# Kernel tuning notes

Hardware: AMD Instinct MI355X
Metric: run time of the kernel (lower is better)

The kernel has to match this reference:

```python
import jax, jax.numpy as jnp
import numpy as np
import math

D_MODEL, N_HEADS, D_FF = 1024, 16, 4096
D_K = D_MODEL // N_HEADS
B, S = 4, 2048
EPS = 1e-5


def layer_norm(x, gamma, beta):
    mean = jnp.mean(x, axis=-1, keepdims=True)
    var = jnp.mean((x - mean) ** 2, axis=-1, keepdims=True)  # unbiased=False
    return gamma * (x - mean) / jnp.sqrt(var + EPS) + beta


def setup_inputs() -> dict:
    key = jax.random.key(0)
    ks = jax.random.split(key, 7)
    std_attn = math.sqrt(2.0 / (D_MODEL + D_MODEL))
    std_ff1 = math.sqrt(2.0 / (D_MODEL + D_FF))
    std_ff2 = math.sqrt(2.0 / (D_FF + D_MODEL))
    return {
        "x": jax.random.normal(ks[0], (B, S, D_MODEL), jnp.float32),
        "W_q": jax.random.normal(ks[1], (D_MODEL, D_MODEL), jnp.float32) * std_attn,
        "W_k": jax.random.normal(ks[2], (D_MODEL, D_MODEL), jnp.float32) * std_attn,
        "W_v": jax.random.normal(ks[3], (D_MODEL, D_MODEL), jnp.float32) * std_attn,
        "W_o": jax.random.normal(ks[4], (D_MODEL, D_MODEL), jnp.float32) * std_attn,
        "W1": jax.random.normal(ks[5], (D_MODEL, D_FF), jnp.float32) * std_ff1,
        "b1": jnp.zeros((D_FF,), jnp.float32),
        "W2": jax.random.normal(ks[6], (D_FF, D_MODEL), jnp.float32) * std_ff2,
        "b2": jnp.zeros((D_MODEL,), jnp.float32),
        "ln1_gamma": jnp.ones((D_MODEL,), jnp.float32),
        "ln1_beta": jnp.zeros((D_MODEL,), jnp.float32),
        "ln2_gamma": jnp.ones((D_MODEL,), jnp.float32),
        "ln2_beta": jnp.zeros((D_MODEL,), jnp.float32),
    }


def reference(x, W_q, W_k, W_v, W_o, W1, b1, W2, b2,
              ln1_gamma, ln1_beta, ln2_gamma, ln2_beta):
    b, s, d = x.shape
    # pre-LN attention block
    ln1 = layer_norm(x, ln1_gamma, ln1_beta)
    q = (ln1 @ W_q).reshape(b, s, N_HEADS, D_K)
    k = (ln1 @ W_k).reshape(b, s, N_HEADS, D_K)
    v = (ln1 @ W_v).reshape(b, s, N_HEADS, D_K)
    scores = jnp.einsum("bqhd,bkhd->bhqk", q, k) / math.sqrt(D_K)
    attn = jax.nn.softmax(scores, axis=-1)
    ctx = jnp.einsum("bhqk,bkhd->bqhd", attn, v).reshape(b, s, d)
    attn_out = ctx @ W_o
    attn_residual = x + attn_out
    # pre-LN FFN block
    ln2 = layer_norm(attn_residual, ln2_gamma, ln2_beta)
    ff = jax.nn.relu(ln2 @ W1 + b1) @ W2 + b2
    return attn_residual + ff
```

## Files before the change

kernel.cpp:

```cpp
#include <hip/hip_runtime.h>
#include <hip/hip_bf16.h>

typedef __attribute__((ext_vector_type(4)))  float  floatx4;
typedef __attribute__((ext_vector_type(16))) float  floatx16;
typedef __attribute__((ext_vector_type(8)))  short  shortx8;
typedef __attribute__((ext_vector_type(4)))  short  shortx4;

__device__ __forceinline__ short f2bf(float f) {
    unsigned u = __float_as_uint(f);
    u += 0x7fffu + ((u >> 16) & 1u);
    return (short)(u >> 16);
}
__device__ __forceinline__ float bf2f(short s) {
    return __uint_as_float(((unsigned)(unsigned short)s) << 16);
}
__device__ __forceinline__ float fast_exp2(float x) {
#if __has_builtin(__builtin_amdgcn_exp2f)
    return __builtin_amdgcn_exp2f(x);
#else
    return exp2f(x);
#endif
}

__device__ __forceinline__ void load_lds16(const void* g, void* l) {
    __builtin_amdgcn_global_load_lds(
        (const __attribute__((address_space(1))) unsigned int*)g,
        (__attribute__((address_space(3))) unsigned int*)l,
        16, 0, 0);
}

__global__ __launch_bounds__(256)
void transpose_w(const float* __restrict__ src, short* __restrict__ dst, int K, int N)
{
    __shared__ __align__(16) float tile[32][33];
    const int n0 = blockIdx.x * 32, k0 = blockIdx.y * 32;
    const int tx = threadIdx.x & 31, ty = threadIdx.x >> 5;
    for (int i = 0; i < 32; i += 8)
        tile[ty + i][tx] = src[(size_t)(k0 + ty + i) * N + n0 + tx];
    __syncthreads();
    for (int i = 0; i < 32; i += 8)
        dst[(size_t)(n0 + ty + i) * K + k0 + tx] = f2bf(tile[tx][ty + i]);
}

__global__ __launch_bounds__(256)
void ln_bf16(const float* __restrict__ x, const float* __restrict__ g,
             const float* __restrict__ be, short* __restrict__ out)
{
    const int row = blockIdx.x;
    const int tid = threadIdx.x;
    const float4 v = reinterpret_cast<const float4*>(x + (size_t)row * 1024)[tid];
    float s  = v.x + v.y + v.z + v.w;
    float ss = v.x * v.x + v.y * v.y + v.z * v.z + v.w * v.w;
    for (int off = 32; off > 0; off >>= 1) {
        s  += __shfl_down(s,  off);
        ss += __shfl_down(ss, off);
    }
    __shared__ float rs[4], rss[4];
    const int wave = tid >> 6, lane = tid & 63;
    if (lane == 0) { rs[wave] = s; rss[wave] = ss; }
    __syncthreads();
    const float S    = rs[0] + rs[1] + rs[2] + rs[3];
    const float SS   = rss[0] + rss[1] + rss[2] + rss[3];
    const float mean = S * (1.0f / 1024.0f);
    const float var  = SS * (1.0f / 1024.0f) - mean * mean;
    const float rstd = rsqrtf(var + 1e-5f);
    const float4 gg = reinterpret_cast<const float4*>(g)[tid];
    const float4 bb = reinterpret_cast<const float4*>(be)[tid];
    shortx4 o;
    o[0] = f2bf(gg.x * ((v.x - mean) * rstd) + bb.x);
    o[1] = f2bf(gg.y * ((v.y - mean) * rstd) + bb.y);
    o[2] = f2bf(gg.z * ((v.z - mean) * rstd) + bb.z);
    o[3] = f2bf(gg.w * ((v.w - mean) * rstd) + bb.w);
    *reinterpret_cast<shortx4*>(out + (size_t)row * 1024 + tid * 4) = o;
}

template <int EPI>
__global__ __launch_bounds__(256)
void gemm_bt(const short* __restrict__ A, const short* __restrict__ Bt,
             short* __restrict__ Cb, float* __restrict__ Cf,
             const float* __restrict__ bias, const float* __restrict__ resid,
             int M, int N, int K)
{
    __shared__ __align__(16) short As[128 * 32];
    __shared__ __align__(16) short Bs[128 * 32];
    const int tid  = threadIdx.x;
    const int wave = tid >> 6;
    const int lane = tid & 63;
    const int quad = lane >> 4;
    const int l16  = lane & 15;
    const int wm = wave >> 1, wn = wave & 1;
    const size_t bm = (size_t)blockIdx.y * 128;
    const size_t bn = (size_t)blockIdx.x * 128;

    floatx4 acc[4][4];
    for (int i = 0; i < 4; i++)
        for (int j = 0; j < 4; j++)
            acc[i][j] = (floatx4){0.f, 0.f, 0.f, 0.f};

    const int c0 = wave * 2, c1 = wave * 2 + 1;
    const int rA0 = c0 * 16 + (lane >> 2);
    const int rA1 = c1 * 16 + (lane >> 2);
    const int colOff = (lane & 3) * 8;

    for (int k0 = 0; k0 < K; k0 += 32) {
        load_lds16(A  + (bm + rA0) * (size_t)K + k0 + colOff, &As[c0 * 512]);
        load_lds16(A  + (bm + rA1) * (size_t)K + k0 + colOff, &As[c1 * 512]);
        load_lds16(Bt + (bn + rA0) * (size_t)K + k0 + colOff, &Bs[c0 * 512]);
        load_lds16(Bt + (bn + rA1) * (size_t)K + k0 + colOff, &Bs[c1 * 512]);
        __syncthreads();
        shortx8 af[4], bf[4];
        for (int mi = 0; mi < 4; mi++)
            af[mi] = *(const shortx8*)&As[(wm * 64 + mi * 16 + l16) * 32 + quad * 8];
        for (int ni = 0; ni < 4; ni++)
            bf[ni] = *(const shortx8*)&Bs[(wn * 64 + ni * 16 + l16) * 32 + quad * 8];
        for (int mi = 0; mi < 4; mi++)
            for (int ni = 0; ni < 4; ni++)
                acc[mi][ni] = __builtin_amdgcn_mfma_f32_16x16x32_bf16(
                    af[mi], bf[ni], acc[mi][ni], 0, 0, 0);
        __syncthreads();
    }

    for (int mi = 0; mi < 4; mi++) {
        for (int ni = 0; ni < 4; ni++) {
            const size_t row0 = bm + wm * 64 + mi * 16 + quad * 4;
            const size_t col  = bn + wn * 64 + ni * 16 + l16;
            for (int r = 0; r < 4; r++) {
                float v = acc[mi][ni][r];
                const size_t idx = (row0 + r) * (size_t)N + col;
                if (EPI == 0) {
                    Cb[idx] = f2bf(v);
                } else if (EPI == 1) {
                    v += bias[col];
                    Cb[idx] = f2bf(v > 0.f ? v : 0.f);
                } else if (EPI == 2) {
                    Cf[idx] = resid[idx] + v;
                } else {
                    v += bias[col];
                    Cf[idx] = resid[idx] + v;
                }
            }
        }
    }
}

__global__ __launch_bounds__(256)
void transpose_v(const short* __restrict__ qkv, short* __restrict__ vt)
{
    __shared__ __align__(16) short tile[64][65];
    const int st = blockIdx.x, h = blockIdx.y, b = blockIdx.z;
    const int t = threadIdx.x;
    for (int i = 0; i < 2; i++) {
        const int idx = i * 256 + t;
        const int s = idx >> 3, dg = idx & 7;
        shortx8 val = *(const shortx8*)&qkv[(size_t)(b * 2048 + st * 64 + s) * 3072
                                           + 2048 + h * 64 + dg * 8];
        for (int u = 0; u < 8; u++) tile[s][dg * 8 + u] = val[u];
    }
    __syncthreads();
    const int d = t >> 2, sg = (t & 3) * 16;
    shortx8 lo, hi;
    for (int i = 0; i < 8; i++) {
        lo[i] = tile[sg + i][d];
        hi[i] = tile[sg + 8 + i][d];
    }
    const size_t base = ((size_t)(b * 16 + h) * 64 + d) * 2048 + st * 64 + sg;
    *(shortx8*)&vt[base]     = lo;
    *(shortx8*)&vt[base + 8] = hi;
}

__global__ __launch_bounds__(512, 4)
void attention_kernel(const short* __restrict__ qkv, const short* __restrict__ vt,
                      short* __restrict__ ctx)
{
    const int qt = blockIdx.x, h = blockIdx.y, b = blockIdx.z;
    const int tid  = threadIdx.x;
    const int wave = tid >> 6;
    const int lane = tid & 63;
    const int l32  = lane & 31;
    const int hf   = lane >> 5;

    __shared__ __align__(16) short Ks[64 * 72];
    __shared__ __align__(16) short Vs[64 * 72];
    __shared__ __align__(16) short Ps[8][32 * 72];

    const int q0 = qt * 256 + wave * 32;
    const float qscale = 0.125f * 1.44269504088896f;
    const short* qrow = qkv + (size_t)(b * 2048 + q0 + l32) * 3072 + h * 64;
    shortx8 qf[4];
    for (int dk = 0; dk < 4; dk++) {
        shortx8 raw = *(const shortx8*)&qrow[dk * 16 + hf * 8];
        for (int j = 0; j < 8; j++) raw[j] = f2bf(bf2f(raw[j]) * qscale);
        qf[dk] = raw;
    }

    floatx16 accO[2];
    for (int t = 0; t < 2; t++)
        for (int r = 0; r < 16; r++) accO[t][r] = 0.f;
    float lsum = 0.f;

    const short* kbase = qkv + (size_t)(b * 2048) * 3072 + 1024 + h * 64;
    const short* vbase = vt + ((size_t)(b * 16 + h) * 64) * 2048;
    short* const psw = &Ps[wave][0];
    unsigned* const pswd = (unsigned*)psw;

    const int ss = tid >> 3, sdg = tid & 7;

    for (int kt = 0; kt < 32; ++kt) {
        __syncthreads();
        {
            shortx8 kv = *(const shortx8*)&kbase[(size_t)(kt * 64 + ss) * 3072 + sdg * 8];
            *(shortx8*)&Ks[ss * 72 + sdg * 8] = kv;
            shortx8 vv = *(const shortx8*)&vbase[(size_t)ss * 2048 + kt * 64 + sdg * 8];
            *(shortx8*)&Vs[ss * 72 + sdg * 8] = vv;
        }
        __syncthreads();

        for (int t = 0; t < 2; t++) {
            floatx16 c;
            for (int r = 0; r < 16; r++) c[r] = 0.f;
            for (int dk = 0; dk < 4; dk++) {
                shortx8 kf = *(const shortx8*)&Ks[(t * 32 + l32) * 72 + dk * 16 + hf * 8];
                c = __builtin_amdgcn_mfma_f32_32x32x16_bf16(kf, qf[dk], c, 0, 0, 0);
            }
            for (int R = 0; R < 4; R++) {
                float2 a, bb;
                a.x  = fast_exp2(c[4 * R + 0]);
                a.y  = fast_exp2(c[4 * R + 1]);
                bb.x = fast_exp2(c[4 * R + 2]);
                bb.y = fast_exp2(c[4 * R + 3]);
                lsum += (a.x + a.y) + (bb.x + bb.y);
                union { __hip_bfloat162 h2[2]; uint2 u; } pk;
                pk.h2[0] = __float22bfloat162_rn(a);
                pk.h2[1] = __float22bfloat162_rn(bb);
                *(uint2*)&pswd[l32 * 36 + t * 16 + 4 * R + 2 * hf] = pk.u;
            }
        }
        asm volatile("s_waitcnt lgkmcnt(0)" ::: "memory");

        shortx8 pf[4];
        for (int sk = 0; sk < 4; sk++)
            pf[sk] = *(const shortx8*)&psw[l32 * 72 + sk * 16 + hf * 8];

        for (int t = 0; t < 2; t++) {
            floatx16 c = accO[t];
            for (int sk = 0; sk < 4; sk++) {
                shortx8 vf = *(const shortx8*)&Vs[(t * 32 + l32) * 72 + sk * 16 + hf * 8];
                c = __builtin_amdgcn_mfma_f32_32x32x16_bf16(vf, pf[sk], c, 0, 0, 0);
            }
            accO[t] = c;
        }
    }

    const float lfull = lsum + __shfl_xor(lsum, 32);
    const float inv = 1.0f / lfull;
    const size_t crow = (size_t)(b * 2048 + q0 + l32) * 1024 + h * 64;
    for (int t = 0; t < 2; t++)
        for (int R = 0; R < 4; R++) {
            float2 a, bb;
            a.x  = accO[t][4 * R + 0] * inv;
            a.y  = accO[t][4 * R + 1] * inv;
            bb.x = accO[t][4 * R + 2] * inv;
            bb.y = accO[t][4 * R + 3] * inv;
            union { __hip_bfloat162 h2[2]; uint2 u; } pk;
            pk.h2[0] = __float22bfloat162_rn(a);
            pk.h2[1] = __float22bfloat162_rn(bb);
            *(uint2*)&ctx[crow + t * 32 + 8 * R + 4 * hf] = pk.u;
        }
}

extern "C" void kernel_launch(void* const* d_in, const int* in_sizes, int n_in,
                              void* d_out, int out_size, void* d_ws, size_t ws_size,
                              hipStream_t stream)
{
    const float* x   = (const float*)d_in[0];
    const float* Wq  = (const float*)d_in[1];
    const float* Wk  = (const float*)d_in[2];
    const float* Wv  = (const float*)d_in[3];
    const float* Wo  = (const float*)d_in[4];
    const float* W1  = (const float*)d_in[5];
    const float* b1  = (const float*)d_in[6];
    const float* W2  = (const float*)d_in[7];
    const float* b2  = (const float*)d_in[8];
    const float* g1  = (const float*)d_in[9];
    const float* be1 = (const float*)d_in[10];
    const float* g2  = (const float*)d_in[11];
    const float* be2 = (const float*)d_in[12];
    float* out = (float*)d_out;
    char*  ws  = (char*)d_ws;

    const size_t MiB = 1u << 20;
    short* regA   = (short*)(ws);
    short* qkv    = (short*)(ws + 16 * MiB);
    short* vt     = (short*)(ws + 64 * MiB);
    short* ff1    = qkv;
    short* Wqkv_t = (short*)(ws + 80 * MiB);
    short* Wo_t   = (short*)(ws + 86 * MiB);
    short* W1_t   = (short*)(ws + 88 * MiB);
    short* W2_t   = (short*)(ws + 96 * MiB);

    const dim3 blk(256);

    transpose_w<<<dim3(32, 32),  blk, 0, stream>>>(Wq, Wqkv_t,                  1024, 1024);
    transpose_w<<<dim3(32, 32),  blk, 0, stream>>>(Wk, Wqkv_t + 1024 * 1024,    1024, 1024);
    transpose_w<<<dim3(32, 32),  blk, 0, stream>>>(Wv, Wqkv_t + 2 * 1024 * 1024,1024, 1024);
    transpose_w<<<dim3(32, 32),  blk, 0, stream>>>(Wo, Wo_t,                    1024, 1024);
    transpose_w<<<dim3(128, 32), blk, 0, stream>>>(W1, W1_t,                    1024, 4096);
    transpose_w<<<dim3(32, 128), blk, 0, stream>>>(W2, W2_t,                    4096, 1024);

    ln_bf16<<<8192, blk, 0, stream>>>(x, g1, be1, regA);
    gemm_bt<0><<<dim3(24, 64), blk, 0, stream>>>(regA, Wqkv_t, qkv, nullptr, nullptr, nullptr,
                                                 8192, 3072, 1024);
    transpose_v<<<dim3(32, 16, 4), blk, 0, stream>>>(qkv, vt);
    attention_kernel<<<dim3(8, 16, 4), dim3(512), 0, stream>>>(qkv, vt, regA);
    gemm_bt<2><<<dim3(8, 64), blk, 0, stream>>>(regA, Wo_t, nullptr, out, nullptr, x,
                                                8192, 1024, 1024);
    ln_bf16<<<8192, blk, 0, stream>>>(out, g2, be2, regA);
    gemm_bt<1><<<dim3(32, 64), blk, 0, stream>>>(regA, W1_t, ff1, nullptr, b1, nullptr,
                                                 8192, 4096, 1024);
    gemm_bt<3><<<dim3(8, 64), blk, 0, stream>>>(ff1, W2_t, nullptr, out, b2, out,
                                                8192, 1024, 4096);
}
```

Baseline: 573.0 us.

## Replace 128x128 GEMM with 256x256 double-buffered swizzled MFMA kernel

Replaces the simple 128x128, K=32 single-buffered GEMM with a 256x256 tile, K=64, 512-thread kernel. It uses double-buffered dynamic LDS of 128 KiB, an XOR-swizzled LDS layout, interleaved prefetch of the next K-tile between MFMA phases, s_setprio around the MFMA blocks, and an XCD-aware workgroup remap. The goal is more data reuse per tile, overlap of global loads with MFMA work, and fewer LDS bank conflicts. In exchange it needs heavy register and LDS use, and grids are small for the N=1024 GEMMs (128 blocks), which risks leaving CUs idle.

New measurement: 552.3 us. 1.04x faster.

```diff
diff --git a/kernel.cpp b/kernel.cpp
--- a/kernel.cpp
+++ b/kernel.cpp
@@ -74,57 +74,171 @@
     *reinterpret_cast<shortx4*>(out + (size_t)row * 1024 + tid * 4) = o;
 }
 
+__device__ __forceinline__ floatx4 mfma2(shortx8 a0, shortx8 a1,
+                                         shortx8 b0, shortx8 b1, floatx4 c) {
+    c = __builtin_amdgcn_mfma_f32_16x16x32_bf16(a0, b0, c, 0, 0, 0);
+    return __builtin_amdgcn_mfma_f32_16x16x32_bf16(a1, b1, c, 0, 0, 0);
+}
+
 template <int EPI>
-__global__ __launch_bounds__(256)
-void gemm_bt(const short* __restrict__ A, const short* __restrict__ Bt,
+__global__ __launch_bounds__(512, 2)
+void gemm256(const short* __restrict__ A, const short* __restrict__ Bt,
              short* __restrict__ Cb, float* __restrict__ Cf,
              const float* __restrict__ bias, const float* __restrict__ resid,
-             int M, int N, int K)
-{
-    __shared__ __align__(16) short As[128 * 32];
-    __shared__ __align__(16) short Bs[128 * 32];
+             int M, int N, int K, int tilesN)
+{
+    extern __shared__ __align__(16) short lds[];
+    short* const As0 = lds;
+    short* const Bs0 = lds + 16384;
+    short* const As1 = lds + 32768;
+    short* const Bs1 = lds + 49152;
+
+    int wg = blockIdx.x;
+    {
+        const int nwg = gridDim.x;
+        const int q = nwg >> 3, r = nwg & 7;
+        const int xcd = wg & 7, loc = wg >> 3;
+        wg = (xcd < r ? xcd * (q + 1) : r * (q + 1) + (xcd - r) * q) + loc;
+    }
+    const int tm = wg / tilesN, tn = wg - tm * tilesN;
+    const size_t bm = (size_t)tm * 256, bn = (size_t)tn * 256;
+
     const int tid  = threadIdx.x;
     const int wave = tid >> 6;
     const int lane = tid & 63;
     const int quad = lane >> 4;
     const int l16  = lane & 15;
-    const int wm = wave >> 1, wn = wave & 1;
-    const size_t bm = (size_t)blockIdx.y * 128;
-    const size_t bn = (size_t)blockIdx.x * 128;
-
-    floatx4 acc[4][4];
-    for (int i = 0; i < 4; i++)
+    const int wm   = wave >> 2;
+    const int wn   = wave & 3;
+
+    const int x7  = l16 & 7;
+    const int go0 = ((quad    ) ^ x7) * 8;
+    const int go1 = ((quad + 4) ^ x7) * 8;
+    const int aoff = (wm * 128 + l16) * 64;
+    const int boff = (wn *  64 + l16) * 64;
+
+    const int rcall = tid >> 3;
+    const int gl    = (tid & 7) ^ (rcall & 7);
+    const short* srcA = A  + (bm + rcall) * (size_t)K + gl * 8;
+    const short* srcB = Bt + (bn + rcall) * (size_t)K + gl * 8;
+    const int dstw = wave * 512;
+
+#define STG(dst, src, c, k0) \
+    load_lds16((src) + (size_t)(c) * 64 * K + (k0), (dst) + (c) * 4096 + dstw)
+
+    const int NT = K >> 6;
+
+    STG(As0, srcA, 0, 0); STG(As0, srcA, 2, 0);
+    STG(Bs0, srcB, 0, 0); STG(Bs0, srcB, 1, 0);
+    STG(Bs0, srcB, 2, 0); STG(Bs0, srcB, 3, 0);
+    STG(As0, srcA, 1, 0); STG(As0, srcA, 3, 0);
+
+    floatx4 acc[8][4];
+#pragma unroll
+    for (int i = 0; i < 8; i++)
+#pragma unroll
         for (int j = 0; j < 4; j++)
             acc[i][j] = (floatx4){0.f, 0.f, 0.f, 0.f};
 
-    const int c0 = wave * 2, c1 = wave * 2 + 1;
-    const int rA0 = c0 * 16 + (lane >> 2);
-    const int rA1 = c1 * 16 + (lane >> 2);
-    const int colOff = (lane & 3) * 8;
-
-    for (int k0 = 0; k0 < K; k0 += 32) {
-        load_lds16(A  + (bm + rA0) * (size_t)K + k0 + colOff, &As[c0 * 512]);
-        load_lds16(A  + (bm + rA1) * (size_t)K + k0 + colOff, &As[c1 * 512]);
-        load_lds16(Bt + (bn + rA0) * (size_t)K + k0 + colOff, &Bs[c0 * 512]);
-        load_lds16(Bt + (bn + rA1) * (size_t)K + k0 + colOff, &Bs[c1 * 512]);
-        __syncthreads();
-        shortx8 af[4], bf[4];
-        for (int mi = 0; mi < 4; mi++)
-            af[mi] = *(const shortx8*)&As[(wm * 64 + mi * 16 + l16) * 32 + quad * 8];
-        for (int ni = 0; ni < 4; ni++)
-            bf[ni] = *(const shortx8*)&Bs[(wn * 64 + ni * 16 + l16) * 32 + quad * 8];
-        for (int mi = 0; mi < 4; mi++)
-            for (int ni = 0; ni < 4; ni++)
-                acc[mi][ni] = __builtin_amdgcn_mfma_f32_16x16x32_bf16(
-                    af[mi], bf[ni], acc[mi][ni], 0, 0, 0);
-        __syncthreads();
-    }
-
-    for (int mi = 0; mi < 4; mi++) {
-        for (int ni = 0; ni < 4; ni++) {
-            const size_t row0 = bm + wm * 64 + mi * 16 + quad * 4;
+    asm volatile("s_waitcnt vmcnt(2)" ::: "memory");
+    __builtin_amdgcn_s_barrier();
+
+    for (int t = 0; t < NT; ++t) {
+        const short* Asc = (t & 1) ? As1 : As0;
+        const short* Bsc = (t & 1) ? Bs1 : Bs0;
+        short* Asn = (t & 1) ? As0 : As1;
+        short* Bsn = (t & 1) ? Bs0 : Bs1;
+        const int kn = (t + 1) << 6;
+        const bool pf = (t + 1) < NT;
+
+        shortx8 aF[4][2], bF[2][2];
+
+#pragma unroll
+        for (int mi = 0; mi < 4; ++mi) {
+            aF[mi][0] = *(const shortx8*)&Asc[aoff + mi * 1024 + go0];
+            aF[mi][1] = *(const shortx8*)&Asc[aoff + mi * 1024 + go1];
+        }
+#pragma unroll
+        for (int ni = 0; ni < 2; ++ni) {
+            bF[ni][0] = *(const shortx8*)&Bsc[boff + ni * 1024 + go0];
+            bF[ni][1] = *(const shortx8*)&Bsc[boff + ni * 1024 + go1];
+        }
+        if (pf) { STG(Asn, srcA, 0, kn); STG(Asn, srcA, 2, kn); }
+        __builtin_amdgcn_s_barrier();
+        asm volatile("s_waitcnt lgkmcnt(0)" ::: "memory");
+        __builtin_amdgcn_s_setprio(1);
+#pragma unroll
+        for (int mi = 0; mi < 4; ++mi)
+#pragma unroll
+            for (int ni = 0; ni < 2; ++ni)
+                acc[mi][ni] = mfma2(aF[mi][0], aF[mi][1], bF[ni][0], bF[ni][1], acc[mi][ni]);
+        __builtin_amdgcn_s_setprio(0);
+        __builtin_amdgcn_s_barrier();
+
+#pragma unroll
+        for (int ni = 0; ni < 2; ++ni) {
+            bF[ni][0] = *(const shortx8*)&Bsc[boff + (ni + 2) * 1024 + go0];
+            bF[ni][1] = *(const shortx8*)&Bsc[boff + (ni + 2) * 1024 + go1];
+        }
+        if (pf) { STG(Bsn, srcB, 0, kn); STG(Bsn, srcB, 1, kn); }
+        __builtin_amdgcn_s_barrier();
+        asm volatile("s_waitcnt lgkmcnt(0)" ::: "memory");
+        __builtin_amdgcn_s_setprio(1);
+#pragma unroll
+        for (int mi = 0; mi < 4; ++mi)
+#pragma unroll
+            for (int ni = 0; ni < 2; ++ni)
+                acc[mi][ni + 2] = mfma2(aF[mi][0], aF[mi][1], bF[ni][0], bF[ni][1], acc[mi][ni + 2]);
+        __builtin_amdgcn_s_setprio(0);
+        if (pf) asm volatile("s_waitcnt vmcnt(4)" ::: "memory");
+        else    asm volatile("s_waitcnt vmcnt(0)" ::: "memory");
+        __builtin_amdgcn_s_barrier();
+
+#pragma unroll
+        for (int mi = 0; mi < 4; ++mi) {
+            aF[mi][0] = *(const shortx8*)&Asc[aoff + (mi + 4) * 1024 + go0];
+            aF[mi][1] = *(const shortx8*)&Asc[aoff + (mi + 4) * 1024 + go1];
+        }
+        if (pf) { STG(Bsn, srcB, 2, kn); STG(Bsn, srcB, 3, kn); }
+        __builtin_amdgcn_s_barrier();
+        asm volatile("s_waitcnt lgkmcnt(0)" ::: "memory");
+        __builtin_amdgcn_s_setprio(1);
+#pragma unroll
+        for (int mi = 0; mi < 4; ++mi)
+#pragma unroll
+            for (int ni = 0; ni < 2; ++ni)
+                acc[mi + 4][ni + 2] = mfma2(aF[mi][0], aF[mi][1], bF[ni][0], bF[ni][1], acc[mi + 4][ni + 2]);
+        __builtin_amdgcn_s_setprio(0);
+        __builtin_amdgcn_s_barrier();
+
+#pragma unroll
+        for (int ni = 0; ni < 2; ++ni) {
+            bF[ni][0] = *(const shortx8*)&Bsc[boff + ni * 1024 + go0];
+            bF[ni][1] = *(const shortx8*)&Bsc[boff + ni * 1024 + go1];
+        }
+        if (pf) { STG(Asn, srcA, 1, kn); STG(Asn, srcA, 3, kn); }
+        __builtin_amdgcn_s_barrier();
+        asm volatile("s_waitcnt lgkmcnt(0)" ::: "memory");
+        __builtin_amdgcn_s_setprio(1);
+#pragma unroll
+        for (int mi = 0; mi < 4; ++mi)
+#pragma unroll
+            for (int ni = 0; ni < 2; ++ni)
+                acc[mi + 4][ni] = mfma2(aF[mi][0], aF[mi][1], bF[ni][0], bF[ni][1], acc[mi + 4][ni]);
+        __builtin_amdgcn_s_setprio(0);
+        asm volatile("s_waitcnt vmcnt(2)" ::: "memory");
+        __builtin_amdgcn_s_barrier();
+    }
+#undef STG
+
+#pragma unroll
+    for (int mi = 0; mi < 8; ++mi) {
+#pragma unroll
+        for (int ni = 0; ni < 4; ++ni) {
+            const size_t row0 = bm + wm * 128 + mi * 16 + quad * 4;
             const size_t col  = bn + wn * 64 + ni * 16 + l16;
-            for (int r = 0; r < 4; r++) {
+#pragma unroll
+            for (int r = 0; r < 4; ++r) {
                 float v = acc[mi][ni][r];
                 const size_t idx = (row0 + r) * (size_t)N + col;
                 if (EPI == 0) {
@@ -299,6 +413,20 @@
     short* W2_t   = (short*)(ws + 96 * MiB);
 
     const dim3 blk(256);
+    const unsigned LDSB = 131072;
+
+    static int attr_once = []() {
+        hipFuncSetAttribute(reinterpret_cast<const void*>(gemm256<0>),
+                            hipFuncAttributeMaxDynamicSharedMemorySize, 131072);
+        hipFuncSetAttribute(reinterpret_cast<const void*>(gemm256<1>),
+                            hipFuncAttributeMaxDynamicSharedMemorySize, 131072);
+        hipFuncSetAttribute(reinterpret_cast<const void*>(gemm256<2>),
+                            hipFuncAttributeMaxDynamicSharedMemorySize, 131072);
+        hipFuncSetAttribute(reinterpret_cast<const void*>(gemm256<3>),
+                            hipFuncAttributeMaxDynamicSharedMemorySize, 131072);
+        return 0;
+    }();
+    (void)attr_once;
 
     transpose_w<<<dim3(32, 32),  blk, 0, stream>>>(Wq, Wqkv_t,                  1024, 1024);
     transpose_w<<<dim3(32, 32),  blk, 0, stream>>>(Wk, Wqkv_t + 1024 * 1024,    1024, 1024);
@@ -308,15 +436,15 @@
     transpose_w<<<dim3(32, 128), blk, 0, stream>>>(W2, W2_t,                    4096, 1024);
 
     ln_bf16<<<8192, blk, 0, stream>>>(x, g1, be1, regA);
-    gemm_bt<0><<<dim3(24, 64), blk, 0, stream>>>(regA, Wqkv_t, qkv, nullptr, nullptr, nullptr,
-                                                 8192, 3072, 1024);
+    gemm256<0><<<dim3(384), dim3(512), LDSB, stream>>>(regA, Wqkv_t, qkv, nullptr,
+                                                       nullptr, nullptr, 8192, 3072, 1024, 12);
     transpose_v<<<dim3(32, 16, 4), blk, 0, stream>>>(qkv, vt);
     attention_kernel<<<dim3(8, 16, 4), dim3(512), 0, stream>>>(qkv, vt, regA);
-    gemm_bt<2><<<dim3(8, 64), blk, 0, stream>>>(regA, Wo_t, nullptr, out, nullptr, x,
-                                                8192, 1024, 1024);
+    gemm256<2><<<dim3(128), dim3(512), LDSB, stream>>>(regA, Wo_t, nullptr, out,
+                                                       nullptr, x, 8192, 1024, 1024, 4);
     ln_bf16<<<8192, blk, 0, stream>>>(out, g2, be2, regA);
-    gemm_bt<1><<<dim3(32, 64), blk, 0, stream>>>(regA, W1_t, ff1, nullptr, b1, nullptr,
-                                                 8192, 4096, 1024);
-    gemm_bt<3><<<dim3(8, 64), blk, 0, stream>>>(ff1, W2_t, nullptr, out, b2, out,
-                                                8192, 1024, 4096);
-}
+    gemm256<1><<<dim3(512), dim3(512), LDSB, stream>>>(regA, W1_t, ff1, nullptr,
+                                                       b1, nullptr, 8192, 4096, 1024, 16);
+    gemm256<3><<<dim3(128), dim3(512), LDSB, stream>>>(ff1, W2_t, nullptr, out,
+                                                       b2, out, 8192, 1024, 4096, 4);
+}
```

## Add split-K with atomics, XCD-aware tile remap, and LDS swizzle to GEMMs

Applied to the files above, without the earlier changes.

The GEMM launch becomes a 1D grid remapped so that consecutive tiles land on the same XCD. The N=1024 GEMMs (Wo and W2) use split-K=2 and accumulate into a zeroed fp32 output with atomicAdd; the residual or bias is added by split 0 only. The LDS tile gets an XOR swizzle to reduce bank conflicts, and launch bounds plus unroll pragmas are added. Split-K raises the workgroup count for the narrow GEMMs, at the cost of a zero-fill pass, atomic traffic and non-deterministic fp32 summation order.

Measured after the change: 589.6 us. 1.03x slower.

```diff
diff --git a/kernel.cpp b/kernel.cpp
--- a/kernel.cpp
+++ b/kernel.cpp
@@ -40,6 +40,13 @@
     __syncthreads();
     for (int i = 0; i < 32; i += 8)
         dst[(size_t)(n0 + ty + i) * K + k0 + tx] = f2bf(tile[tx][ty + i]);
+}
+
+__global__ __launch_bounds__(256)
+void zero_f32(float* __restrict__ p)
+{
+    const size_t i = (size_t)blockIdx.x * 256 + threadIdx.x;
+    reinterpret_cast<float4*>(p)[i] = make_float4(0.f, 0.f, 0.f, 0.f);
 }
 
 __global__ __launch_bounds__(256)
@@ -75,55 +82,80 @@
 }
 
 template <int EPI>
-__global__ __launch_bounds__(256)
+__global__ __launch_bounds__(256, 4)
 void gemm_bt(const short* __restrict__ A, const short* __restrict__ Bt,
              short* __restrict__ Cb, float* __restrict__ Cf,
              const float* __restrict__ bias, const float* __restrict__ resid,
-             int M, int N, int K)
+             int M, int N, int K, int tilesN, int nsplit)
 {
     __shared__ __align__(16) short As[128 * 32];
     __shared__ __align__(16) short Bs[128 * 32];
+
+    int wg = blockIdx.x;
+    {
+        const int nwg = gridDim.x;
+        const int q = nwg >> 3, r = nwg & 7;
+        const int xcd = wg & 7, loc = wg >> 3;
+        wg = (xcd < r ? xcd * (q + 1) : r * (q + 1) + (xcd - r) * q) + loc;
+    }
+    const int ntiles = gridDim.x / nsplit;
+    const int sp   = wg / ntiles;
+    const int tile = wg - sp * ntiles;
+    const int tm = tile / tilesN, tn = tile - tm * tilesN;
+    const size_t bm = (size_t)tm * 128, bn = (size_t)tn * 128;
+    const int Ks   = K / nsplit;
+    const int kbeg = sp * Ks;
+
     const int tid  = threadIdx.x;
     const int wave = tid >> 6;
     const int lane = tid & 63;
     const int quad = lane >> 4;
     const int l16  = lane & 15;
     const int wm = wave >> 1, wn = wave & 1;
-    const size_t bm = (size_t)blockIdx.y * 128;
-    const size_t bn = (size_t)blockIdx.x * 128;
 
     floatx4 acc[4][4];
+#pragma unroll
     for (int i = 0; i < 4; i++)
+#pragma unroll
         for (int j = 0; j < 4; j++)
             acc[i][j] = (floatx4){0.f, 0.f, 0.f, 0.f};
 
     const int c0 = wave * 2, c1 = wave * 2 + 1;
     const int rA0 = c0 * 16 + (lane >> 2);
     const int rA1 = c1 * 16 + (lane >> 2);
-    const int colOff = (lane & 3) * 8;
-
-    for (int k0 = 0; k0 < K; k0 += 32) {
+    const int colOff = ((lane & 3) ^ ((lane >> 3) & 3)) * 8;
+
+    const int g0 = (quad ^ ((l16 >> 1) & 3)) * 8;
+
+    for (int k0 = kbeg; k0 < kbeg + Ks; k0 += 32) {
         load_lds16(A  + (bm + rA0) * (size_t)K + k0 + colOff, &As[c0 * 512]);
         load_lds16(A  + (bm + rA1) * (size_t)K + k0 + colOff, &As[c1 * 512]);
         load_lds16(Bt + (bn + rA0) * (size_t)K + k0 + colOff, &Bs[c0 * 512]);
         load_lds16(Bt + (bn + rA1) * (size_t)K + k0 + colOff, &Bs[c1 * 512]);
         __syncthreads();
         shortx8 af[4], bf[4];
+#pragma unroll
         for (int mi = 0; mi < 4; mi++)
-            af[mi] = *(const shortx8*)&As[(wm * 64 + mi * 16 + l16) * 32 + quad * 8];
+            af[mi] = *(const shortx8*)&As[(wm * 64 + mi * 16 + l16) * 32 + g0];
+#pragma unroll
         for (int ni = 0; ni < 4; ni++)
-            bf[ni] = *(const shortx8*)&Bs[(wn * 64 + ni * 16 + l16) * 32 + quad * 8];
+            bf[ni] = *(const shortx8*)&Bs[(wn * 64 + ni * 16 + l16) * 32 + g0];
+#pragma unroll
         for (int mi = 0; mi < 4; mi++)
+#pragma unroll
             for (int ni = 0; ni < 4; ni++)
                 acc[mi][ni] = __builtin_amdgcn_mfma_f32_16x16x32_bf16(
                     af[mi], bf[ni], acc[mi][ni], 0, 0, 0);
         __syncthreads();
     }
 
+#pragma unroll
     for (int mi = 0; mi < 4; mi++) {
+#pragma unroll
         for (int ni = 0; ni < 4; ni++) {
             const size_t row0 = bm + wm * 64 + mi * 16 + quad * 4;
             const size_t col  = bn + wn * 64 + ni * 16 + l16;
+#pragma unroll
             for (int r = 0; r < 4; r++) {
                 float v = acc[mi][ni][r];
                 const size_t idx = (row0 + r) * (size_t)N + col;
@@ -134,9 +166,12 @@
                     Cb[idx] = f2bf(v > 0.f ? v : 0.f);
                 } else if (EPI == 2) {
                     Cf[idx] = resid[idx] + v;
+                } else if (EPI == 4) {
+                    if (sp == 0) v += bias[col];
+                    atomicAdd(&Cf[idx], v);
                 } else {
-                    v += bias[col];
-                    Cf[idx] = resid[idx] + v;
+                    if (sp == 0) v += resid[idx];
+                    atomicAdd(&Cf[idx], v);
                 }
             }
         }
@@ -308,15 +343,16 @@
     transpose_w<<<dim3(32, 128), blk, 0, stream>>>(W2, W2_t,                    4096, 1024);
 
     ln_bf16<<<8192, blk, 0, stream>>>(x, g1, be1, regA);
-    gemm_bt<0><<<dim3(24, 64), blk, 0, stream>>>(regA, Wqkv_t, qkv, nullptr, nullptr, nullptr,
-                                                 8192, 3072, 1024);
+    gemm_bt<0><<<dim3(1536), blk, 0, stream>>>(regA, Wqkv_t, qkv, nullptr,
+                                               nullptr, nullptr, 8192, 3072, 1024, 24, 1);
     transpose_v<<<dim3(32, 16, 4), blk, 0, stream>>>(qkv, vt);
     attention_kernel<<<dim3(8, 16, 4), dim3(512), 0, stream>>>(qkv, vt, regA);
-    gemm_bt<2><<<dim3(8, 64), blk, 0, stream>>>(regA, Wo_t, nullptr, out, nullptr, x,
-                                                8192, 1024, 1024);
+    zero_f32<<<dim3(8192), blk, 0, stream>>>(out);
+    gemm_bt<5><<<dim3(1024), blk, 0, stream>>>(regA, Wo_t, nullptr, out,
+                                               nullptr, x, 8192, 1024, 1024, 8, 2);
     ln_bf16<<<8192, blk, 0, stream>>>(out, g2, be2, regA);
-    gemm_bt<1><<<dim3(32, 64), blk, 0, stream>>>(regA, W1_t, ff1, nullptr, b1, nullptr,
-                                                 8192, 4096, 1024);
-    gemm_bt<3><<<dim3(8, 64), blk, 0, stream>>>(ff1, W2_t, nullptr, out, b2, out,
-                                                8192, 1024, 4096);
-}
+    gemm_bt<1><<<dim3(2048), blk, 0, stream>>>(regA, W1_t, ff1, nullptr,
+                                               b1, nullptr, 8192, 4096, 1024, 32, 1);
+    gemm_bt<4><<<dim3(1024), blk, 0, stream>>>(ff1, W2_t, nullptr, out,
+                                               b2, nullptr, 8192, 1024, 4096, 8, 2);
+}
```
